# Kernel optimization log

Hardware: AMD Instinct MI355X
Metric: run time of the kernel (lower is better)

Reference implementation:

```python
import jax, jax.numpy as jnp
import numpy as np

N, D, M, H, FF, L = 8192, 14, 36, 256, 2048, 2  # rows, d_model, material feats, mlp hidden, ffn, layers
EPS = 1e-5


def _ln(x, g, b):
    mu = jnp.mean(x, axis=-1, keepdims=True)
    var = jnp.mean((x - mu) ** 2, axis=-1, keepdims=True)
    return (x - mu) * jax.lax.rsqrt(var + EPS) * g + b


def setup_inputs() -> dict:
    key = jax.random.key(0)
    ks = iter(jax.random.split(key, 32))
    p = lambda shape, fan: jax.random.normal(next(ks), shape, jnp.float32) * (fan ** -0.5)
    return {
        "x": jax.random.normal(next(ks), (N, D), jnp.float32),
        "y": jax.random.normal(next(ks), (N, M), jnp.float32),
        # 2 post-LN TransformerEncoderLayers (nhead=1, dim_feedforward=2048, relu)
        "attn_wqkv": p((L, 3 * D, D), D), "attn_bqkv": p((L, 3 * D), D),
        "attn_wo": p((L, D, D), D), "attn_bo": p((L, D), D),
        "ln1_g": jnp.ones((L, D)), "ln1_b": jnp.zeros((L, D)),
        "ff_w1": p((L, FF, D), D), "ff_b1": p((L, FF), D),
        "ff_w2": p((L, D, FF), FF), "ff_b2": p((L, D), FF),
        "ln2_g": jnp.ones((L, D)), "ln2_b": jnp.zeros((L, D)),
        "fc1_w": p((D, D), D), "fc1_b": p((D,), D),
        "fc2_w": p((1, D), D), "fc2_b": p((1,), D),
        "fc3_w": p((H, D + M + 1), D + M + 1), "fc3_b": p((H,), D + M + 1),
        "fc4_w": p((H, H), H), "fc4_b": p((H,), H),
        "fc5_w": p((1, H), H), "fc5_b": p((1,), H),
    }


def reference(x, y, attn_wqkv, attn_bqkv, attn_wo, attn_bo, ln1_g, ln1_b,
              ff_w1, ff_b1, ff_w2, ff_b2, ln2_g, ln2_b,
              fc1_w, fc1_b, fc2_w, fc2_b, fc3_w, fc3_b, fc4_w, fc4_b, fc5_w, fc5_b):
    h = x  # [N, D]; batch of size 1 squeezed away
    for l in range(L):
        qkv = h @ attn_wqkv[l].T + attn_bqkv[l]            # [N, 3D]
        q, k, v = jnp.split(qkv, 3, axis=-1)
        scores = (q @ k.T) * (D ** -0.5)                   # [N, N]
        a = jax.nn.softmax(scores, axis=-1) @ v            # [N, D]
        a = a @ attn_wo[l].T + attn_bo[l]
        h = _ln(h + a, ln1_g[l], ln1_b[l])
        f = jax.nn.relu(h @ ff_w1[l].T + ff_b1[l]) @ ff_w2[l].T + ff_b2[l]
        h = _ln(h + f, ln2_g[l], ln2_b[l])
    x1 = h @ fc1_w.T + fc1_b                               # [N, D]
    size_out = (x1 @ fc2_w.T + fc2_b)[:, 0]                # [N]

    # batched replacement of the per-row python loop
    size_int = size_out.astype(jnp.int32)                  # trunc toward zero, like .int()
    size_f = size_int.astype(jnp.float32)[:, None]         # [N, 1]
    reg_in = jnp.concatenate([size_f, x, y], axis=1)       # [N, 1+D+M]
    r = jax.nn.relu(reg_in @ fc3_w.T + fc3_b)
    r = jax.nn.relu(r @ fc4_w.T + fc4_b)
    reg_values = (r @ fc5_w.T + fc5_b)[:, 0]               # [N]
    reg_values = jnp.where(size_int != 0, reg_values, 0.0)
    return size_out, reg_values
```

## Files before the change

### kernel.cpp

```cpp
#include <hip/hip_runtime.h>
#include <math.h>

#define NN 8192
#define DD 14
#define DP 16
#define FF 2048
#define HID 256
#define LN_EPS 1e-5f
#define NCH 16
#define NFCH 8
#define QSCALE (1.4426950408889634f / 3.7416573867739413f)

typedef short bf16x8 __attribute__((ext_vector_type(8)));
typedef float f32x4 __attribute__((ext_vector_type(4)));

#define LOAD16(dst, srcp) { \
  const float4* _p = (const float4*)(srcp); \
  float4 _a = _p[0], _b = _p[1], _c = _p[2], _d = _p[3]; \
  dst[0]=_a.x; dst[1]=_a.y; dst[2]=_a.z; dst[3]=_a.w; \
  dst[4]=_b.x; dst[5]=_b.y; dst[6]=_b.z; dst[7]=_b.w; \
  dst[8]=_c.x; dst[9]=_c.y; dst[10]=_c.z; dst[11]=_c.w; \
  dst[12]=_d.x; dst[13]=_d.y; dst[14]=_d.z; dst[15]=_d.w; }

#define STORE16(dstp, src) { \
  float4* _p = (float4*)(dstp); \
  _p[0] = make_float4(src[0], src[1], src[2], src[3]); \
  _p[1] = make_float4(src[4], src[5], src[6], src[7]); \
  _p[2] = make_float4(src[8], src[9], src[10], src[11]); \
  _p[3] = make_float4(src[12], src[13], src[14], src[15]); }

static __device__ __forceinline__ float fast_exp2(float x) {
#if __has_builtin(__builtin_amdgcn_exp2f)
  return __builtin_amdgcn_exp2f(x);
#else
  return exp2f(x);
#endif
}

static __device__ __forceinline__ unsigned short bf_hi(float x) {
  return (unsigned short)(__float_as_uint(x) >> 16);
}
static __device__ __forceinline__ float bf_hi_f(float x) {
  return __uint_as_float(__float_as_uint(x) & 0xffff0000u);
}

static __device__ __forceinline__ void qkv_compute_store(
    int r, const float* hr, const float* __restrict__ wqkv,
    const float* __restrict__ bqkv, unsigned int* __restrict__ Qpack,
    unsigned int* __restrict__ KB1, unsigned int* __restrict__ KB2,
    unsigned short* __restrict__ VhiT, unsigned short* __restrict__ VloT) {
  float q[14], k[14], v[14];
  #pragma unroll 6
  for (int c = 0; c < 42; c++) {
    const float* w = wqkv + c * 14;
    float s = bqkv[c];
    #pragma unroll
    for (int d = 0; d < 14; d++) s = fmaf(hr[d], w[d], s);
    if (c < 14)       q[c] = s * QSCALE;
    else if (c < 28)  k[c - 14] = s;
    else              v[c - 28] = s;
  }
  unsigned int qp[16], k1[16], k2[16];
  unsigned short qh[14], ql[14], kh[14], kl[14];
  #pragma unroll
  for (int d = 0; d < 14; d++) {
    qh[d] = bf_hi(q[d]);
    ql[d] = bf_hi(q[d] - bf_hi_f(q[d]));
    kh[d] = bf_hi(k[d]);
    kl[d] = bf_hi(k[d] - bf_hi_f(k[d]));
  }
  #pragma unroll
  for (int i = 0; i < 7; i++) {
    qp[i]     = (unsigned int)qh[2*i] | ((unsigned int)qh[2*i+1] << 16);
    qp[8 + i] = (unsigned int)ql[2*i] | ((unsigned int)ql[2*i+1] << 16);
    k1[i]     = (unsigned int)kh[2*i] | ((unsigned int)kh[2*i+1] << 16);
    k1[8 + i] = k1[i];
    k2[i]     = (unsigned int)kl[2*i] | ((unsigned int)kl[2*i+1] << 16);
    k2[8 + i] = k2[i];
  }
  qp[7] = 0; qp[15] = 0; k1[7] = 0; k1[15] = 0; k2[7] = 0; k2[15] = 0;
  uint4* Qp4 = (uint4*)(Qpack + (size_t)r * 16);
  uint4* K14 = (uint4*)(KB1 + (size_t)r * 16);
  uint4* K24 = (uint4*)(KB2 + (size_t)r * 16);
  #pragma unroll
  for (int i = 0; i < 4; i++) {
    Qp4[i] = make_uint4(qp[4*i], qp[4*i+1], qp[4*i+2], qp[4*i+3]);
    K14[i] = make_uint4(k1[4*i], k1[4*i+1], k1[4*i+2], k1[4*i+3]);
    K24[i] = make_uint4(k2[4*i], k2[4*i+1], k2[4*i+2], k2[4*i+3]);
  }
  #pragma unroll
  for (int d = 0; d < 14; d++) {
    VhiT[(size_t)d * NN + r] = bf_hi(v[d]);
    VloT[(size_t)d * NN + r] = bf_hi(v[d] - bf_hi_f(v[d]));
  }
  VhiT[(size_t)14 * NN + r] = 0x3F80;
  VhiT[(size_t)15 * NN + r] = 0;
  VloT[(size_t)14 * NN + r] = 0;
  VloT[(size_t)15 * NN + r] = 0;
}

static __device__ __forceinline__ void store_apack(unsigned int* dst, const float* o) {
  unsigned int qp[16];
  unsigned short hh[14], ll[14];
  #pragma unroll
  for (int d = 0; d < 14; d++) {
    hh[d] = bf_hi(o[d]);
    ll[d] = bf_hi(o[d] - bf_hi_f(o[d]));
  }
  #pragma unroll
  for (int i = 0; i < 7; i++) {
    qp[i]     = (unsigned int)hh[2*i] | ((unsigned int)hh[2*i+1] << 16);
    qp[8 + i] = (unsigned int)ll[2*i] | ((unsigned int)ll[2*i+1] << 16);
  }
  qp[7] = 0; qp[15] = 0;
  uint4* d4 = (uint4*)dst;
  #pragma unroll
  for (int i = 0; i < 4; i++)
    d4[i] = make_uint4(qp[4*i], qp[4*i+1], qp[4*i+2], qp[4*i+3]);
}

__global__ void pack_weights(const float* __restrict__ w3, const float* __restrict__ w4,
                             const float* __restrict__ ffw1, const float* __restrict__ ffw2,
                             unsigned short* __restrict__ B3h, unsigned short* __restrict__ B3l,
                             unsigned short* __restrict__ B4h, unsigned short* __restrict__ B4l,
                             unsigned int* __restrict__ W1B1, unsigned int* __restrict__ W1B2,
                             unsigned short* __restrict__ W2h, unsigned short* __restrict__ W2l) {
  const int blk = blockIdx.x, tid = threadIdx.x;
  if (blk < 32) {
    int t = blk * 256 + tid;
    int lane = t & 63, ks = (t >> 6) & 7, nt = t >> 9;
    int n = nt * 16 + (lane & 15);
    int k0 = ks * 32 + (lane >> 4) * 8;
    unsigned int h4[4], l4[4];
    #pragma unroll
    for (int jj = 0; jj < 4; jj++) {
      unsigned short h2[2], l2[2];
      #pragma unroll
      for (int e = 0; e < 2; e++) {
        float v = w4[(size_t)n * 256 + k0 + jj * 2 + e];
        h2[e] = bf_hi(v);
        l2[e] = bf_hi(v - bf_hi_f(v));
      }
      h4[jj] = (unsigned int)h2[0] | ((unsigned int)h2[1] << 16);
      l4[jj] = (unsigned int)l2[0] | ((unsigned int)l2[1] << 16);
    }
    ((uint4*)B4h)[t] = make_uint4(h4[0], h4[1], h4[2], h4[3]);
    ((uint4*)B4l)[t] = make_uint4(l4[0], l4[1], l4[2], l4[3]);
    if (ks < 2) {
      int fi = (nt * 2 + ks) * 64 + lane;
      #pragma unroll
      for (int jj = 0; jj < 4; jj++) {
        unsigned short h2[2], l2[2];
        #pragma unroll
        for (int e = 0; e < 2; e++) {
          int k = k0 + jj * 2 + e;
          float v = (k < 51) ? w3[(size_t)n * 51 + k] : 0.f;
          h2[e] = bf_hi(v);
          l2[e] = bf_hi(v - bf_hi_f(v));
        }
        h4[jj] = (unsigned int)h2[0] | ((unsigned int)h2[1] << 16);
        l4[jj] = (unsigned int)l2[0] | ((unsigned int)l2[1] << 16);
      }
      ((uint4*)B3h)[fi] = make_uint4(h4[0], h4[1], h4[2], h4[3]);
      ((uint4*)B3l)[fi] = make_uint4(l4[0], l4[1], l4[2], l4[3]);
    }
  } else if (blk < 48) {
    int t = (blk - 32) * 256 + tid;
    int l = t >> 11, j = t & 2047;
    const float* wrow = ffw1 + ((size_t)l * FF + j) * 14;
    unsigned int k1[16], k2[16];
    unsigned short kh[14], kl[14];
    #pragma unroll
    for (int d = 0; d < 14; d++) {
      float v = wrow[d];
      kh[d] = bf_hi(v);
      kl[d] = bf_hi(v - bf_hi_f(v));
    }
    #pragma unroll
    for (int i = 0; i < 7; i++) {
      k1[i] = (unsigned int)kh[2*i] | ((unsigned int)kh[2*i+1] << 16);
      k1[8 + i] = k1[i];
      k2[i] = (unsigned int)kl[2*i] | ((unsigned int)kl[2*i+1] << 16);
      k2[8 + i] = k2[i];
    }
    k1[7] = 0; k1[15] = 0; k2[7] = 0; k2[15] = 0;
    uint4* d1 = (uint4*)(W1B1 + (size_t)t * 16);
    uint4* d2 = (uint4*)(W1B2 + (size_t)t * 16);
    #pragma unroll
    for (int i = 0; i < 4; i++) {
      d1[i] = make_uint4(k1[4*i], k1[4*i+1], k1[4*i+2], k1[4*i+3]);
      d2[i] = make_uint4(k2[4*i], k2[4*i+1], k2[4*i+2], k2[4*i+3]);
    }
  } else {
    int t = (blk - 48) * 256 + tid;
    int l = t >> 11, j = t & 2047;
    #pragma unroll
    for (int d = 0; d < 16; d++) {
      float v = (d < 14) ? ffw2[((size_t)l * 14 + d) * FF + j] : 0.f;
      W2h[((size_t)l * 16 + d) * FF + j] = bf_hi(v);
      W2l[((size_t)l * 16 + d) * FF + j] = bf_hi(v - bf_hi_f(v));
    }
  }
}

__global__ void qkv_pack_x(const float* __restrict__ x, const float* __restrict__ wqkv,
                           const float* __restrict__ bqkv, float* __restrict__ h,
                           unsigned int* __restrict__ Qpack,
                           unsigned int* __restrict__ KB1, unsigned int* __restrict__ KB2,
                           unsigned short* __restrict__ VhiT,
                           unsigned short* __restrict__ VloT) {
  int r = blockIdx.x * 64 + threadIdx.x;
  float hr[16];
  #pragma unroll
  for (int d = 0; d < 14; d++) hr[d] = x[(size_t)r * 14 + d];
  hr[14] = 0.f; hr[15] = 0.f;
  STORE16(h + (size_t)r * DP, hr);
  qkv_compute_store(r, hr, wqkv, bqkv, Qpack, KB1, KB2, VhiT, VloT);
}

__global__ __launch_bounds__(256, 4) void attn_mfma(
    const unsigned int* __restrict__ Qpack, const unsigned int* __restrict__ KB1,
    const unsigned int* __restrict__ KB2, const unsigned short* __restrict__ VhiT,
    const unsigned short* __restrict__ VloT, float* __restrict__ part) {
  __shared__ float Plds[4][16][36];
  const int tid = threadIdx.x;
  const int wave = tid >> 6;
  const int lane = tid & 63;
  const int lo4 = lane & 15;
  const int hi4 = lane >> 4;
  const int qbase = blockIdx.x * 128 + wave * 32;
  const int kbase0 = blockIdx.y * 512;

  const bf16x8* Qp = (const bf16x8*)Qpack;
  const bf16x8* B1 = (const bf16x8*)KB1;
  const bf16x8* B2 = (const bf16x8*)KB2;
  const bf16x8* Vh = (const bf16x8*)VhiT;
  const bf16x8* Vl = (const bf16x8*)VloT;

  bf16x8 aQ0 = Qp[(size_t)(qbase + lo4) * 4 + hi4];
  bf16x8 aQ1 = Qp[(size_t)(qbase + 16 + lo4) * 4 + hi4];
  f32x4 acc0 = {0.f, 0.f, 0.f, 0.f};
  f32x4 acc1 = {0.f, 0.f, 0.f, 0.f};
  const f32x4 zero = {0.f, 0.f, 0.f, 0.f};

  for (int c = 0; c < 16; c++) {
    const int kb = kbase0 + c * 32;
    bf16x8 b1g0 = B1[(size_t)(kb + lo4) * 4 + hi4];
    bf16x8 b2g0 = B2[(size_t)(kb + lo4) * 4 + hi4];
    bf16x8 b1g1 = B1[(size_t)(kb + 16 + lo4) * 4 + hi4];
    bf16x8 b2g1 = B2[(size_t)(kb + 16 + lo4) * 4 + hi4];
    bf16x8 vh = Vh[(size_t)lo4 * 1024 + (kb >> 3) + hi4];
    bf16x8 vl = Vl[(size_t)lo4 * 1024 + (kb >> 3) + hi4];

    #pragma unroll
    for (int sub = 0; sub < 2; sub++) {
      bf16x8 aQ = sub ? aQ1 : aQ0;
      f32x4 s0 = __builtin_amdgcn_mfma_f32_16x16x32_bf16(aQ, b1g0, zero, 0, 0, 0);
      s0 = __builtin_amdgcn_mfma_f32_16x16x32_bf16(aQ, b2g0, s0, 0, 0, 0);
      f32x4 s1 = __builtin_amdgcn_mfma_f32_16x16x32_bf16(aQ, b1g1, zero, 0, 0, 0);
      s1 = __builtin_amdgcn_mfma_f32_16x16x32_bf16(aQ, b2g1, s1, 0, 0, 0);
      #pragma unroll
      for (int reg = 0; reg < 4; reg++) {
        Plds[wave][hi4 * 4 + reg][lo4]      = fast_exp2(s0[reg]);
        Plds[wave][hi4 * 4 + reg][16 + lo4] = fast_exp2(s1[reg]);
      }
      __asm__ volatile("s_waitcnt lgkmcnt(0)" ::: "memory");
      const float4* pr = (const float4*)&Plds[wave][lo4][hi4 * 8];
      float4 f0 = pr[0];
      float4 f1 = pr[1];
      float pv[8] = {f0.x, f0.y, f0.z, f0.w, f1.x, f1.y, f1.z, f1.w};
      bf16x8 ph, pl;
      #pragma unroll
      for (int i = 0; i < 8; i++) {
        unsigned int u = __float_as_uint(pv[i]);
        ph[i] = (short)(u >> 16);
        float rr = pv[i] - __uint_as_float(u & 0xffff0000u);
        pl[i] = (short)(__float_as_uint(rr) >> 16);
      }
      f32x4 acc = sub ? acc1 : acc0;
      acc = __builtin_amdgcn_mfma_f32_16x16x32_bf16(ph, vh, acc, 0, 0, 0);
      acc = __builtin_amdgcn_mfma_f32_16x16x32_bf16(pl, vh, acc, 0, 0, 0);
      acc = __builtin_amdgcn_mfma_f32_16x16x32_bf16(ph, vl, acc, 0, 0, 0);
      if (sub) acc1 = acc; else acc0 = acc;
      __asm__ volatile("s_waitcnt lgkmcnt(0)" ::: "memory");
    }
  }
  float* pbase = part + (size_t)blockIdx.y * NN * 16;
  #pragma unroll
  for (int reg = 0; reg < 4; reg++) {
    int row0 = qbase + hi4 * 4 + reg;
    pbase[(size_t)row0 * 16 + lo4] = acc0[reg];
    pbase[(size_t)(row0 + 16) * 16 + lo4] = acc1[reg];
  }
}

__global__ void attn_comb_ln1(float* __restrict__ h, const float* __restrict__ part,
                              const float* __restrict__ wo, const float* __restrict__ bo,
                              const float* __restrict__ g, const float* __restrict__ b,
                              unsigned int* __restrict__ Hpack) {
  int r = blockIdx.x * 64 + threadIdx.x;
  float L = 0.f;
  float A[14];
  #pragma unroll
  for (int d = 0; d < 14; d++) A[d] = 0.f;
  for (int c = 0; c < NCH; c++) {
    float p[16];
    LOAD16(p, part + ((size_t)c * NN + r) * 16);
    L += p[14];
    #pragma unroll
    for (int d = 0; d < 14; d++) A[d] += p[d];
  }
  float inv = 1.f / L;
  float a[14];
  #pragma unroll
  for (int d = 0; d < 14; d++) a[d] = A[d] * inv;
  float hr[16];
  LOAD16(hr, h + (size_t)r * DP);
  float xx[14];
  #pragma unroll
  for (int i = 0; i < 14; i++) {
    float s = bo[i];
    #pragma unroll
    for (int d = 0; d < 14; d++) s = fmaf(wo[i * 14 + d], a[d], s);
    xx[i] = hr[i] + s;
  }
  float mu = 0.f;
  #pragma unroll
  for (int i = 0; i < 14; i++) mu += xx[i];
  mu *= (1.f / 14.f);
  float var = 0.f;
  #pragma unroll
  for (int i = 0; i < 14; i++) { float t = xx[i] - mu; var = fmaf(t, t, var); }
  var *= (1.f / 14.f);
  float rs = rsqrtf(var + LN_EPS);
  float o[16];
  #pragma unroll
  for (int i = 0; i < 14; i++) o[i] = fmaf((xx[i] - mu) * rs, g[i], b[i]);
  o[14] = 0.f; o[15] = 0.f;
  STORE16(h + (size_t)r * DP, o);
  store_apack(Hpack + (size_t)r * 16, o);
}

__global__ __launch_bounds__(256, 4) void ffn_mfma(
    const unsigned int* __restrict__ Hpack, const unsigned int* __restrict__ W1B1,
    const unsigned int* __restrict__ W1B2, const unsigned short* __restrict__ W2h,
    const unsigned short* __restrict__ W2l, const float* __restrict__ b1,
    float* __restrict__ part) {
  __shared__ float Plds[4][16][36];
  const int tid = threadIdx.x;
  const int wave = tid >> 6;
  const int lane = tid & 63;
  const int lo4 = lane & 15;
  const int hi4 = lane >> 4;
  const int qbase = blockIdx.x * 128 + wave * 32;
  const int jbase0 = blockIdx.y * 256;

  const bf16x8* Hp = (const bf16x8*)Hpack;
  const bf16x8* B1 = (const bf16x8*)W1B1;
  const bf16x8* B2 = (const bf16x8*)W1B2;
  const bf16x8* Vh = (const bf16x8*)W2h;
  const bf16x8* Vl = (const bf16x8*)W2l;

  bf16x8 aH0 = Hp[(size_t)(qbase + lo4) * 4 + hi4];
  bf16x8 aH1 = Hp[(size_t)(qbase + 16 + lo4) * 4 + hi4];
  f32x4 acc0 = {0.f, 0.f, 0.f, 0.f};
  f32x4 acc1 = {0.f, 0.f, 0.f, 0.f};
  const f32x4 zero = {0.f, 0.f, 0.f, 0.f};

  for (int c = 0; c < 8; c++) {
    const int jb = jbase0 + c * 32;
    bf16x8 b1g0 = B1[(size_t)(jb + lo4) * 4 + hi4];
    bf16x8 b2g0 = B2[(size_t)(jb + lo4) * 4 + hi4];
    bf16x8 b1g1 = B1[(size_t)(jb + 16 + lo4) * 4 + hi4];
    bf16x8 b2g1 = B2[(size_t)(jb + 16 + lo4) * 4 + hi4];
    bf16x8 vh = Vh[(size_t)lo4 * 256 + (jb >> 3) + hi4];
    bf16x8 vl = Vl[(size_t)lo4 * 256 + (jb >> 3) + hi4];
    float bb0 = b1[jb + lo4];
    float bb1 = b1[jb + 16 + lo4];

    #pragma unroll
    for (int sub = 0; sub < 2; sub++) {
      bf16x8 aH = sub ? aH1 : aH0;
      f32x4 s0 = __builtin_amdgcn_mfma_f32_16x16x32_bf16(aH, b1g0, zero, 0, 0, 0);
      s0 = __builtin_amdgcn_mfma_f32_16x16x32_bf16(aH, b2g0, s0, 0, 0, 0);
      f32x4 s1 = __builtin_amdgcn_mfma_f32_16x16x32_bf16(aH, b1g1, zero, 0, 0, 0);
      s1 = __builtin_amdgcn_mfma_f32_16x16x32_bf16(aH, b2g1, s1, 0, 0, 0);
      #pragma unroll
      for (int reg = 0; reg < 4; reg++) {
        Plds[wave][hi4 * 4 + reg][lo4]      = fmaxf(s0[reg] + bb0, 0.f);
        Plds[wave][hi4 * 4 + reg][16 + lo4] = fmaxf(s1[reg] + bb1, 0.f);
      }
      __asm__ volatile("s_waitcnt lgkmcnt(0)" ::: "memory");
      const float4* pr = (const float4*)&Plds[wave][lo4][hi4 * 8];
      float4 f0 = pr[0];
      float4 f1 = pr[1];
      float pv[8] = {f0.x, f0.y, f0.z, f0.w, f1.x, f1.y, f1.z, f1.w};
      bf16x8 th, tl;
      #pragma unroll
      for (int i = 0; i < 8; i++) {
        unsigned int u = __float_as_uint(pv[i]);
        th[i] = (short)(u >> 16);
        float rr = pv[i] - __uint_as_float(u & 0xffff0000u);
        tl[i] = (short)(__float_as_uint(rr) >> 16);
      }
      f32x4 acc = sub ? acc1 : acc0;
      acc = __builtin_amdgcn_mfma_f32_16x16x32_bf16(th, vh, acc, 0, 0, 0);
      acc = __builtin_amdgcn_mfma_f32_16x16x32_bf16(tl, vh, acc, 0, 0, 0);
      acc = __builtin_amdgcn_mfma_f32_16x16x32_bf16(th, vl, acc, 0, 0, 0);
      if (sub) acc1 = acc; else acc0 = acc;
      __asm__ volatile("s_waitcnt lgkmcnt(0)" ::: "memory");
    }
  }
  float* pbase = part + (size_t)blockIdx.y * NN * 16;
  #pragma unroll
  for (int reg = 0; reg < 4; reg++) {
    int row0 = qbase + hi4 * 4 + reg;
    pbase[(size_t)row0 * 16 + lo4] = acc0[reg];
    pbase[(size_t)(row0 + 16) * 16 + lo4] = acc1[reg];
  }
}

__global__ void ffn_ln2_qkv(float* __restrict__ h, const float* __restrict__ part,
                            const float* __restrict__ b2, const float* __restrict__ g,
                            const float* __restrict__ b,
                            const float* __restrict__ wqkv, const float* __restrict__ bqkv,
                            unsigned int* __restrict__ Qpack,
                            unsigned int* __restrict__ KB1, unsigned int* __restrict__ KB2,
                            unsigned short* __restrict__ VhiT,
                            unsigned short* __restrict__ VloT) {
  int r = blockIdx.x * 64 + threadIdx.x;
  float f[14];
  #pragma unroll
  for (int d = 0; d < 14; d++) f[d] = b2[d];
  for (int c = 0; c < NFCH; c++) {
    float p[16];
    LOAD16(p, part + ((size_t)c * NN + r) * 16);
    #pragma unroll
    for (int d = 0; d < 14; d++) f[d] += p[d];
  }
  float hr[16];
  LOAD16(hr, h + (size_t)r * DP);
  float xx[14];
  #pragma unroll
  for (int i = 0; i < 14; i++) xx[i] = hr[i] + f[i];
  float mu = 0.f;
  #pragma unroll
  for (int i = 0; i < 14; i++) mu += xx[i];
  mu *= (1.f / 14.f);
  float var = 0.f;
  #pragma unroll
  for (int i = 0; i < 14; i++) { float t = xx[i] - mu; var = fmaf(t, t, var); }
  var *= (1.f / 14.f);
  float rs = rsqrtf(var + LN_EPS);
  float o[16];
  #pragma unroll
  for (int i = 0; i < 14; i++) o[i] = fmaf((xx[i] - mu) * rs, g[i], b[i]);
  o[14] = 0.f; o[15] = 0.f;
  STORE16(h + (size_t)r * DP, o);
  qkv_compute_store(r, o, wqkv, bqkv, Qpack, KB1, KB2, VhiT, VloT);
}

__global__ void ffn_ln2_size(const float* __restrict__ h, const float* __restrict__ part,
                             const float* __restrict__ b2, const float* __restrict__ g,
                             const float* __restrict__ b,
                             const float* __restrict__ fc1w, const float* __restrict__ fc1b,
                             const float* __restrict__ fc2w, const float* __restrict__ fc2b,
                             float* __restrict__ out, float* __restrict__ sizef) {
  int r = blockIdx.x * 64 + threadIdx.x;
  float f[14];
  #pragma unroll
  for (int d = 0; d < 14; d++) f[d] = b2[d];
  for (int c = 0; c < NFCH; c++) {
    float p[16];
    LOAD16(p, part + ((size_t)c * NN + r) * 16);
    #pragma unroll
    for (int d = 0; d < 14; d++) f[d] += p[d];
  }
  float hr[16];
  LOAD16(hr, h + (size_t)r * DP);
  float xx[14];
  #pragma unroll
  for (int i = 0; i < 14; i++) xx[i] = hr[i] + f[i];
  float mu = 0.f;
  #pragma unroll
  for (int i = 0; i < 14; i++) mu += xx[i];
  mu *= (1.f / 14.f);
  float var = 0.f;
  #pragma unroll
  for (int i = 0; i < 14; i++) { float t = xx[i] - mu; var = fmaf(t, t, var); }
  var *= (1.f / 14.f);
  float rs = rsqrtf(var + LN_EPS);
  float o[14];
  #pragma unroll
  for (int i = 0; i < 14; i++) o[i] = fmaf((xx[i] - mu) * rs, g[i], b[i]);
  float s = fc2b[0];
  #pragma unroll
  for (int i = 0; i < 14; i++) {
    float t = fc1b[i];
    #pragma unroll
    for (int d = 0; d < 14; d++) t = fmaf(fc1w[i * 14 + d], o[d], t);
    s = fmaf(t, fc2w[i], s);
  }
  out[r] = s;
  int si = (int)s;
  sizef[r] = (float)si;
}

__global__ __launch_bounds__(256, 4) void head_reg_mfma(
    const float* __restrict__ x, const float* __restrict__ y,
    const float* __restrict__ sizef,
    const unsigned short* __restrict__ B3h, const unsigned short* __restrict__ B3l,
    const float* __restrict__ b3,
    const unsigned short* __restrict__ B4h, const unsigned short* __restrict__ B4l,
    const float* __restrict__ b4,
    const float* __restrict__ w5, const float* __restrict__ b5,
    float* __restrict__ outr) {
  __shared__ alignas(16) unsigned short Ah[16][72], Al[16][72];
  __shared__ alignas(16) unsigned short R1h[16][264], R1l[16][264];
  __shared__ float sred[4][16][16];
  const int tid = threadIdx.x;
  const int wave = tid >> 6;
  const int lane = tid & 63;
  const int lo4 = lane & 15;
  const int hi4 = lane >> 4;
  const int rbase = blockIdx.x * 16;

  for (int idx = tid; idx < 16 * 64; idx += 256) {
    int m = idx >> 6, k = idx & 63;
    int r = rbase + m;
    float v = 0.f;
    if (k == 0)       v = sizef[r];
    else if (k < 15)  v = x[(size_t)r * 14 + (k - 1)];
    else if (k < 51)  v = y[(size_t)r * 36 + (k - 15)];
    Ah[m][k] = bf_hi(v);
    Al[m][k] = bf_hi(v - bf_hi_f(v));
  }
  __syncthreads();

  const f32x4 zero = {0.f, 0.f, 0.f, 0.f};
  f32x4 acc[4];
  #pragma unroll
  for (int nt = 0; nt < 4; nt++) acc[nt] = zero;

  #pragma unroll
  for (int ks = 0; ks < 2; ks++) {
    bf16x8 ah = *(const bf16x8*)&Ah[lo4][ks * 32 + hi4 * 8];
    bf16x8 al = *(const bf16x8*)&Al[lo4][ks * 32 + hi4 * 8];
    #pragma unroll
    for (int nt = 0; nt < 4; nt++) {
      int fi = ((wave * 4 + nt) * 2 + ks) * 64 + lane;
      bf16x8 bh = ((const bf16x8*)B3h)[fi];
      bf16x8 bl = ((const bf16x8*)B3l)[fi];
      acc[nt] = __builtin_amdgcn_mfma_f32_16x16x32_bf16(ah, bh, acc[nt], 0, 0, 0);
      acc[nt] = __builtin_amdgcn_mfma_f32_16x16x32_bf16(al, bh, acc[nt], 0, 0, 0);
      acc[nt] = __builtin_amdgcn_mfma_f32_16x16x32_bf16(ah, bl, acc[nt], 0, 0, 0);
    }
  }
  #pragma unroll
  for (int nt = 0; nt < 4; nt++) {
    int n = (wave * 4 + nt) * 16 + lo4;
    float bb = b3[n];
    #pragma unroll
    for (int reg = 0; reg < 4; reg++) {
      int m = hi4 * 4 + reg;
      float v = fmaxf(acc[nt][reg] + bb, 0.f);
      R1h[m][n] = bf_hi(v);
      R1l[m][n] = bf_hi(v - bf_hi_f(v));
    }
  }
  __syncthreads();

  #pragma unroll
  for (int nt = 0; nt < 4; nt++) acc[nt] = zero;
  #pragma unroll
  for (int ks = 0; ks < 8; ks++) {
    bf16x8 ah = *(const bf16x8*)&R1h[lo4][ks * 32 + hi4 * 8];
    bf16x8 al = *(const bf16x8*)&R1l[lo4][ks * 32 + hi4 * 8];
    #pragma unroll
    for (int nt = 0; nt < 4; nt++) {
      int fi = ((wave * 4 + nt) * 8 + ks) * 64 + lane;
      bf16x8 bh = ((const bf16x8*)B4h)[fi];
      bf16x8 bl = ((const bf16x8*)B4l)[fi];
      acc[nt] = __builtin_amdgcn_mfma_f32_16x16x32_bf16(ah, bh, acc[nt], 0, 0, 0);
      acc[nt] = __builtin_amdgcn_mfma_f32_16x16x32_bf16(al, bh, acc[nt], 0, 0, 0);
      acc[nt] = __builtin_amdgcn_mfma_f32_16x16x32_bf16(ah, bl, acc[nt], 0, 0, 0);
    }
  }
  float s[4] = {0.f, 0.f, 0.f, 0.f};
  #pragma unroll
  for (int nt = 0; nt < 4; nt++) {
    int n = (wave * 4 + nt) * 16 + lo4;
    float bb = b4[n], ww = w5[n];
    #pragma unroll
    for (int reg = 0; reg < 4; reg++)
      s[reg] = fmaf(fmaxf(acc[nt][reg] + bb, 0.f), ww, s[reg]);
  }
  #pragma unroll
  for (int reg = 0; reg < 4; reg++) sred[wave][hi4 * 4 + reg][lo4] = s[reg];
  __syncthreads();

  if (tid < 16) {
    float t = b5[0];
    #pragma unroll
    for (int w = 0; w < 4; w++) {
      const float4* p = (const float4*)&sred[w][tid][0];
      float4 a0 = p[0], a1 = p[1], a2 = p[2], a3 = p[3];
      t += ((a0.x + a0.y) + (a0.z + a0.w)) + ((a1.x + a1.y) + (a1.z + a1.w)) +
           ((a2.x + a2.y) + (a2.z + a2.w)) + ((a3.x + a3.y) + (a3.z + a3.w));
    }
    float sz = sizef[rbase + tid];
    outr[rbase + tid] = (sz != 0.f) ? t : 0.f;
  }
}

extern "C" void kernel_launch(void* const* d_in, const int* in_sizes, int n_in,
                              void* d_out, int out_size, void* d_ws, size_t ws_size,
                              hipStream_t stream) {
  const float* x    = (const float*)d_in[0];
  const float* y    = (const float*)d_in[1];
  const float* wqkv = (const float*)d_in[2];
  const float* bqkv = (const float*)d_in[3];
  const float* wo   = (const float*)d_in[4];
  const float* bo   = (const float*)d_in[5];
  const float* ln1g = (const float*)d_in[6];
  const float* ln1b = (const float*)d_in[7];
  const float* ffw1 = (const float*)d_in[8];
  const float* ffb1 = (const float*)d_in[9];
  const float* ffw2 = (const float*)d_in[10];
  const float* ffb2 = (const float*)d_in[11];
  const float* ln2g = (const float*)d_in[12];
  const float* ln2b = (const float*)d_in[13];
  const float* fc1w = (const float*)d_in[14];
  const float* fc1b = (const float*)d_in[15];
  const float* fc2w = (const float*)d_in[16];
  const float* fc2b = (const float*)d_in[17];
  const float* fc3w = (const float*)d_in[18];
  const float* fc3b = (const float*)d_in[19];
  const float* fc4w = (const float*)d_in[20];
  const float* fc4b = (const float*)d_in[21];
  const float* fc5w = (const float*)d_in[22];
  const float* fc5b = (const float*)d_in[23];

  float* ws = (float*)d_ws;
  float*          h     = ws;
  unsigned int*   Qpack = (unsigned int*)(ws + 131072);
  unsigned int*   KB1   = (unsigned int*)(ws + 262144);
  unsigned int*   KB2   = (unsigned int*)(ws + 393216);
  unsigned short* VhiT  = (unsigned short*)(ws + 524288);
  unsigned short* VloT  = (unsigned short*)(ws + 589824);
  unsigned int*   Hpack = (unsigned int*)(ws + 655360);
  float*          part  = ws + 786432;
  float*          sizef = ws + 2883584;
  unsigned short* B3h   = (unsigned short*)(ws + 2891776);
  unsigned short* B3l   = (unsigned short*)(ws + 2899968);
  unsigned short* B4h   = (unsigned short*)(ws + 2908160);
  unsigned short* B4l   = (unsigned short*)(ws + 2940928);
  unsigned int*   W1B1  = (unsigned int*)(ws + 2973696);
  unsigned int*   W1B2  = (unsigned int*)(ws + 3039232);
  unsigned short* W2h   = (unsigned short*)(ws + 3104768);
  unsigned short* W2l   = (unsigned short*)(ws + 3137536);

  float* out = (float*)d_out;

  pack_weights<<<64, 256, 0, stream>>>(fc3w, fc4w, ffw1, ffw2, B3h, B3l, B4h, B4l,
                                       W1B1, W1B2, W2h, W2l);
  qkv_pack_x<<<128, 64, 0, stream>>>(x, wqkv, bqkv, h, Qpack, KB1, KB2, VhiT, VloT);
  for (int l = 0; l < 2; l++) {
    attn_mfma<<<dim3(64, NCH), 256, 0, stream>>>(Qpack, KB1, KB2, VhiT, VloT, part);
    attn_comb_ln1<<<128, 64, 0, stream>>>(h, part, wo + (size_t)l * 196,
                                          bo + (size_t)l * 14, ln1g + (size_t)l * 14,
                                          ln1b + (size_t)l * 14, Hpack);
    ffn_mfma<<<dim3(64, NFCH), 256, 0, stream>>>(
        Hpack, W1B1 + (size_t)l * 2048 * 16, W1B2 + (size_t)l * 2048 * 16,
        W2h + (size_t)l * 16 * FF, W2l + (size_t)l * 16 * FF,
        ffb1 + (size_t)l * FF, part);
    if (l == 0) {
      ffn_ln2_qkv<<<128, 64, 0, stream>>>(h, part, ffb2, ln2g, ln2b,
                                          wqkv + 42 * 14, bqkv + 42,
                                          Qpack, KB1, KB2, VhiT, VloT);
    } else {
      ffn_ln2_size<<<128, 64, 0, stream>>>(h, part, ffb2 + 14, ln2g + 14, ln2b + 14,
                                           fc1w, fc1b, fc2w, fc2b, out, sizef);
    }
  }
  head_reg_mfma<<<512, 256, 0, stream>>>(x, y, sizef, B3h, B3l, fc3b, B4h, B4l, fc4b,
                                         fc5w, fc5b, out + NN);
}
```

Before: 261.6 us.

## Fuse pack kernels, interleave MFMA sub-tiles, split combine reductions, fuse tail

Merges weight packing with the initial QKV projection into one launch, and fuses the final LN2/size head into the regression head kernel, which removes launches and the sizef round trip through global memory. The attention and FFN inner loops now issue both 16-row sub-tiles' MFMAs together with a larger LDS staging buffer, so independent MFMA chains overlap instead of running in a serial loop. The combine/LN kernels now use four threads per row with shuffle reductions over the partial chunks, giving more parallelism at the cost of idle lanes in the per-row tail. The extra LDS and registers may reduce occupancy.

```diff
diff --git a/kernel.cpp b/kernel.cpp
--- a/kernel.cpp
+++ b/kernel.cpp
@@ -42,6 +42,16 @@
 }
 static __device__ __forceinline__ float bf_hi_f(float x) {
   return __uint_as_float(__float_as_uint(x) & 0xffff0000u);
+}
+
+static __device__ __forceinline__ void split8(const float* pv, bf16x8* ph, bf16x8* pl) {
+  #pragma unroll
+  for (int i = 0; i < 8; i++) {
+    unsigned int u = __float_as_uint(pv[i]);
+    (*ph)[i] = (short)(u >> 16);
+    float rr = pv[i] - __uint_as_float(u & 0xffff0000u);
+    (*pl)[i] = (short)(__float_as_uint(rr) >> 16);
+  }
 }
 
 static __device__ __forceinline__ void qkv_compute_store(
@@ -119,12 +129,17 @@
     d4[i] = make_uint4(qp[4*i], qp[4*i+1], qp[4*i+2], qp[4*i+3]);
 }
 
-__global__ void pack_weights(const float* __restrict__ w3, const float* __restrict__ w4,
-                             const float* __restrict__ ffw1, const float* __restrict__ ffw2,
-                             unsigned short* __restrict__ B3h, unsigned short* __restrict__ B3l,
-                             unsigned short* __restrict__ B4h, unsigned short* __restrict__ B4l,
-                             unsigned int* __restrict__ W1B1, unsigned int* __restrict__ W1B2,
-                             unsigned short* __restrict__ W2h, unsigned short* __restrict__ W2l) {
+__global__ void pack_all(const float* __restrict__ w3, const float* __restrict__ w4,
+                         const float* __restrict__ ffw1, const float* __restrict__ ffw2,
+                         const float* __restrict__ x, const float* __restrict__ wqkv,
+                         const float* __restrict__ bqkv, float* __restrict__ h,
+                         unsigned int* __restrict__ Qpack,
+                         unsigned int* __restrict__ KB1, unsigned int* __restrict__ KB2,
+                         unsigned short* __restrict__ VhiT, unsigned short* __restrict__ VloT,
+                         unsigned short* __restrict__ B3h, unsigned short* __restrict__ B3l,
+                         unsigned short* __restrict__ B4h, unsigned short* __restrict__ B4l,
+                         unsigned int* __restrict__ W1B1, unsigned int* __restrict__ W1B2,
+                         unsigned short* __restrict__ W2h, unsigned short* __restrict__ W2l) {
   const int blk = blockIdx.x, tid = threadIdx.x;
   if (blk < 32) {
     int t = blk * 256 + tid;
@@ -191,7 +206,7 @@
       d1[i] = make_uint4(k1[4*i], k1[4*i+1], k1[4*i+2], k1[4*i+3]);
       d2[i] = make_uint4(k2[4*i], k2[4*i+1], k2[4*i+2], k2[4*i+3]);
     }
-  } else {
+  } else if (blk < 64) {
     int t = (blk - 48) * 256 + tid;
     int l = t >> 11, j = t & 2047;
     #pragma unroll
@@ -200,29 +215,22 @@
       W2h[((size_t)l * 16 + d) * FF + j] = bf_hi(v);
       W2l[((size_t)l * 16 + d) * FF + j] = bf_hi(v - bf_hi_f(v));
     }
-  }
-}
-
-__global__ void qkv_pack_x(const float* __restrict__ x, const float* __restrict__ wqkv,
-                           const float* __restrict__ bqkv, float* __restrict__ h,
-                           unsigned int* __restrict__ Qpack,
-                           unsigned int* __restrict__ KB1, unsigned int* __restrict__ KB2,
-                           unsigned short* __restrict__ VhiT,
-                           unsigned short* __restrict__ VloT) {
-  int r = blockIdx.x * 64 + threadIdx.x;
-  float hr[16];
-  #pragma unroll
-  for (int d = 0; d < 14; d++) hr[d] = x[(size_t)r * 14 + d];
-  hr[14] = 0.f; hr[15] = 0.f;
-  STORE16(h + (size_t)r * DP, hr);
-  qkv_compute_store(r, hr, wqkv, bqkv, Qpack, KB1, KB2, VhiT, VloT);
+  } else {
+    int r = (blk - 64) * 256 + tid;
+    float hr[16];
+    #pragma unroll
+    for (int d = 0; d < 14; d++) hr[d] = x[(size_t)r * 14 + d];
+    hr[14] = 0.f; hr[15] = 0.f;
+    STORE16(h + (size_t)r * DP, hr);
+    qkv_compute_store(r, hr, wqkv, bqkv, Qpack, KB1, KB2, VhiT, VloT);
+  }
 }
 
 __global__ __launch_bounds__(256, 4) void attn_mfma(
     const unsigned int* __restrict__ Qpack, const unsigned int* __restrict__ KB1,
     const unsigned int* __restrict__ KB2, const unsigned short* __restrict__ VhiT,
     const unsigned short* __restrict__ VloT, float* __restrict__ part) {
-  __shared__ float Plds[4][16][36];
+  __shared__ float Plds[4][32][36];
   const int tid = threadIdx.x;
   const int wave = tid >> 6;
   const int lane = tid & 63;
@@ -252,38 +260,37 @@
     bf16x8 vh = Vh[(size_t)lo4 * 1024 + (kb >> 3) + hi4];
     bf16x8 vl = Vl[(size_t)lo4 * 1024 + (kb >> 3) + hi4];
 
-    #pragma unroll
-    for (int sub = 0; sub < 2; sub++) {
-      bf16x8 aQ = sub ? aQ1 : aQ0;
-      f32x4 s0 = __builtin_amdgcn_mfma_f32_16x16x32_bf16(aQ, b1g0, zero, 0, 0, 0);
-      s0 = __builtin_amdgcn_mfma_f32_16x16x32_bf16(aQ, b2g0, s0, 0, 0, 0);
-      f32x4 s1 = __builtin_amdgcn_mfma_f32_16x16x32_bf16(aQ, b1g1, zero, 0, 0, 0);
-      s1 = __builtin_amdgcn_mfma_f32_16x16x32_bf16(aQ, b2g1, s1, 0, 0, 0);
-      #pragma unroll
-      for (int reg = 0; reg < 4; reg++) {
-        Plds[wave][hi4 * 4 + reg][lo4]      = fast_exp2(s0[reg]);
-        Plds[wave][hi4 * 4 + reg][16 + lo4] = fast_exp2(s1[reg]);
-      }
-      __asm__ volatile("s_waitcnt lgkmcnt(0)" ::: "memory");
-      const float4* pr = (const float4*)&Plds[wave][lo4][hi4 * 8];
-      float4 f0 = pr[0];
-      float4 f1 = pr[1];
-      float pv[8] = {f0.x, f0.y, f0.z, f0.w, f1.x, f1.y, f1.z, f1.w};
-      bf16x8 ph, pl;
-      #pragma unroll
-      for (int i = 0; i < 8; i++) {
-        unsigned int u = __float_as_uint(pv[i]);
-        ph[i] = (short)(u >> 16);
-        float rr = pv[i] - __uint_as_float(u & 0xffff0000u);
-        pl[i] = (short)(__float_as_uint(rr) >> 16);
-      }
-      f32x4 acc = sub ? acc1 : acc0;
-      acc = __builtin_amdgcn_mfma_f32_16x16x32_bf16(ph, vh, acc, 0, 0, 0);
-      acc = __builtin_amdgcn_mfma_f32_16x16x32_bf16(pl, vh, acc, 0, 0, 0);
-      acc = __builtin_amdgcn_mfma_f32_16x16x32_bf16(ph, vl, acc, 0, 0, 0);
-      if (sub) acc1 = acc; else acc0 = acc;
-      __asm__ volatile("s_waitcnt lgkmcnt(0)" ::: "memory");
-    }
+    f32x4 s00 = __builtin_amdgcn_mfma_f32_16x16x32_bf16(aQ0, b1g0, zero, 0, 0, 0);
+    f32x4 s01 = __builtin_amdgcn_mfma_f32_16x16x32_bf16(aQ0, b1g1, zero, 0, 0, 0);
+    f32x4 s10 = __builtin_amdgcn_mfma_f32_16x16x32_bf16(aQ1, b1g0, zero, 0, 0, 0);
+    f32x4 s11 = __builtin_amdgcn_mfma_f32_16x16x32_bf16(aQ1, b1g1, zero, 0, 0, 0);
+    s00 = __builtin_amdgcn_mfma_f32_16x16x32_bf16(aQ0, b2g0, s00, 0, 0, 0);
+    s01 = __builtin_amdgcn_mfma_f32_16x16x32_bf16(aQ0, b2g1, s01, 0, 0, 0);
+    s10 = __builtin_amdgcn_mfma_f32_16x16x32_bf16(aQ1, b2g0, s10, 0, 0, 0);
+    s11 = __builtin_amdgcn_mfma_f32_16x16x32_bf16(aQ1, b2g1, s11, 0, 0, 0);
+    #pragma unroll
+    for (int reg = 0; reg < 4; reg++) {
+      Plds[wave][hi4 * 4 + reg][lo4]           = fast_exp2(s00[reg]);
+      Plds[wave][hi4 * 4 + reg][16 + lo4]      = fast_exp2(s01[reg]);
+      Plds[wave][16 + hi4 * 4 + reg][lo4]      = fast_exp2(s10[reg]);
+      Plds[wave][16 + hi4 * 4 + reg][16 + lo4] = fast_exp2(s11[reg]);
+    }
+    __asm__ volatile("s_waitcnt lgkmcnt(0)" ::: "memory");
+    const float4* p0 = (const float4*)&Plds[wave][lo4][hi4 * 8];
+    const float4* p1 = (const float4*)&Plds[wave][16 + lo4][hi4 * 8];
+    float4 a0 = p0[0], a1 = p0[1], c0 = p1[0], c1 = p1[1];
+    float pv0[8] = {a0.x, a0.y, a0.z, a0.w, a1.x, a1.y, a1.z, a1.w};
+    float pv1[8] = {c0.x, c0.y, c0.z, c0.w, c1.x, c1.y, c1.z, c1.w};
+    bf16x8 ph0, pl0, ph1, pl1;
+    split8(pv0, &ph0, &pl0);
+    split8(pv1, &ph1, &pl1);
+    acc0 = __builtin_amdgcn_mfma_f32_16x16x32_bf16(ph0, vh, acc0, 0, 0, 0);
+    acc1 = __builtin_amdgcn_mfma_f32_16x16x32_bf16(ph1, vh, acc1, 0, 0, 0);
+    acc0 = __builtin_amdgcn_mfma_f32_16x16x32_bf16(pl0, vh, acc0, 0, 0, 0);
+    acc1 = __builtin_amdgcn_mfma_f32_16x16x32_bf16(pl1, vh, acc1, 0, 0, 0);
+    acc0 = __builtin_amdgcn_mfma_f32_16x16x32_bf16(ph0, vl, acc0, 0, 0, 0);
+    acc1 = __builtin_amdgcn_mfma_f32_16x16x32_bf16(ph1, vl, acc1, 0, 0, 0);
+    __asm__ volatile("s_waitcnt lgkmcnt(0)" ::: "memory");
   }
   float* pbase = part + (size_t)blockIdx.y * NN * 16;
   #pragma unroll
@@ -298,47 +305,57 @@
                               const float* __restrict__ wo, const float* __restrict__ bo,
                               const float* __restrict__ g, const float* __restrict__ b,
                               unsigned int* __restrict__ Hpack) {
-  int r = blockIdx.x * 64 + threadIdx.x;
+  int t = blockIdx.x * 128 + threadIdx.x;
+  int r = t >> 2, q = t & 3;
   float L = 0.f;
   float A[14];
   #pragma unroll
   for (int d = 0; d < 14; d++) A[d] = 0.f;
-  for (int c = 0; c < NCH; c++) {
+  #pragma unroll
+  for (int c = q; c < NCH; c += 4) {
     float p[16];
     LOAD16(p, part + ((size_t)c * NN + r) * 16);
     L += p[14];
     #pragma unroll
     for (int d = 0; d < 14; d++) A[d] += p[d];
   }
-  float inv = 1.f / L;
-  float a[14];
-  #pragma unroll
-  for (int d = 0; d < 14; d++) a[d] = A[d] * inv;
-  float hr[16];
-  LOAD16(hr, h + (size_t)r * DP);
-  float xx[14];
-  #pragma unroll
-  for (int i = 0; i < 14; i++) {
-    float s = bo[i];
-    #pragma unroll
-    for (int d = 0; d < 14; d++) s = fmaf(wo[i * 14 + d], a[d], s);
-    xx[i] = hr[i] + s;
-  }
-  float mu = 0.f;
-  #pragma unroll
-  for (int i = 0; i < 14; i++) mu += xx[i];
-  mu *= (1.f / 14.f);
-  float var = 0.f;
-  #pragma unroll
-  for (int i = 0; i < 14; i++) { float t = xx[i] - mu; var = fmaf(t, t, var); }
-  var *= (1.f / 14.f);
-  float rs = rsqrtf(var + LN_EPS);
-  float o[16];
-  #pragma unroll
-  for (int i = 0; i < 14; i++) o[i] = fmaf((xx[i] - mu) * rs, g[i], b[i]);
-  o[14] = 0.f; o[15] = 0.f;
-  STORE16(h + (size_t)r * DP, o);
-  store_apack(Hpack + (size_t)r * 16, o);
+  #pragma unroll
+  for (int off = 1; off < 4; off <<= 1) {
+    L += __shfl_xor(L, off, 64);
+    #pragma unroll
+    for (int d = 0; d < 14; d++) A[d] += __shfl_xor(A[d], off, 64);
+  }
+  if (q == 0) {
+    float inv = 1.f / L;
+    float a[14];
+    #pragma unroll
+    for (int d = 0; d < 14; d++) a[d] = A[d] * inv;
+    float hr[16];
+    LOAD16(hr, h + (size_t)r * DP);
+    float xx[14];
+    #pragma unroll
+    for (int i = 0; i < 14; i++) {
+      float s = bo[i];
+      #pragma unroll
+      for (int d = 0; d < 14; d++) s = fmaf(wo[i * 14 + d], a[d], s);
+      xx[i] = hr[i] + s;
+    }
+    float mu = 0.f;
+    #pragma unroll
+    for (int i = 0; i < 14; i++) mu += xx[i];
+    mu *= (1.f / 14.f);
+    float var = 0.f;
+    #pragma unroll
+    for (int i = 0; i < 14; i++) { float tt = xx[i] - mu; var = fmaf(tt, tt, var); }
+    var *= (1.f / 14.f);
+    float rs = rsqrtf(var + LN_EPS);
+    float o[16];
+    #pragma unroll
+    for (int i = 0; i < 14; i++) o[i] = fmaf((xx[i] - mu) * rs, g[i], b[i]);
+    o[14] = 0.f; o[15] = 0.f;
+    STORE16(h + (size_t)r * DP, o);
+    store_apack(Hpack + (size_t)r * 16, o);
+  }
 }
 
 __global__ __launch_bounds__(256, 4) void ffn_mfma(
@@ -346,7 +363,7 @@
     const unsigned int* __restrict__ W1B2, const unsigned short* __restrict__ W2h,
     const unsigned short* __restrict__ W2l, const float* __restrict__ b1,
     float* __restrict__ part) {
-  __shared__ float Plds[4][16][36];
+  __shared__ float Plds[4][32][36];
   const int tid = threadIdx.x;
   const int wave = tid >> 6;
   const int lane = tid & 63;
@@ -378,38 +395,37 @@
     float bb0 = b1[jb + lo4];
     float bb1 = b1[jb + 16 + lo4];
 
-    #pragma unroll
-    for (int sub = 0; sub < 2; sub++) {
-      bf16x8 aH = sub ? aH1 : aH0;
-      f32x4 s0 = __builtin_amdgcn_mfma_f32_16x16x32_bf16(aH, b1g0, zero, 0, 0, 0);
-      s0 = __builtin_amdgcn_mfma_f32_16x16x32_bf16(aH, b2g0, s0, 0, 0, 0);
-      f32x4 s1 = __builtin_amdgcn_mfma_f32_16x16x32_bf16(aH, b1g1, zero, 0, 0, 0);
-      s1 = __builtin_amdgcn_mfma_f32_16x16x32_bf16(aH, b2g1, s1, 0, 0, 0);
-      #pragma unroll
-      for (int reg = 0; reg < 4; reg++) {
-        Plds[wave][hi4 * 4 + reg][lo4]      = fmaxf(s0[reg] + bb0, 0.f);
-        Plds[wave][hi4 * 4 + reg][16 + lo4] = fmaxf(s1[reg] + bb1, 0.f);
-      }
-      __asm__ volatile("s_waitcnt lgkmcnt(0)" ::: "memory");
-      const float4* pr = (const float4*)&Plds[wave][lo4][hi4 * 8];
-      float4 f0 = pr[0];
-      float4 f1 = pr[1];
-      float pv[8] = {f0.x, f0.y, f0.z, f0.w, f1.x, f1.y, f1.z, f1.w};
-      bf16x8 th, tl;
-      #pragma unroll
-      for (int i = 0; i < 8; i++) {
-        unsigned int u = __float_as_uint(pv[i]);
-        th[i] = (short)(u >> 16);
-        float rr = pv[i] - __uint_as_float(u & 0xffff0000u);
-        tl[i] = (short)(__float_as_uint(rr) >> 16);
-      }
-      f32x4 acc = sub ? acc1 : acc0;
-      acc = __builtin_amdgcn_mfma_f32_16x16x32_bf16(th, vh, acc, 0, 0, 0);
-      acc = __builtin_amdgcn_mfma_f32_16x16x32_bf16(tl, vh, acc, 0, 0, 0);
-      acc = __builtin_amdgcn_mfma_f32_16x16x32_bf16(th, vl, acc, 0, 0, 0);
-      if (sub) acc1 = acc; else acc0 = acc;
-      __asm__ volatile("s_waitcnt lgkmcnt(0)" ::: "memory");
-    }
+    f32x4 s00 = __builtin_amdgcn_mfma_f32_16x16x32_bf16(aH0, b1g0, zero, 0, 0, 0);
+    f32x4 s01 = __builtin_amdgcn_mfma_f32_16x16x32_bf16(aH0, b1g1, zero, 0, 0, 0);
+    f32x4 s10 = __builtin_amdgcn_mfma_f32_16x16x32_bf16(aH1, b1g0, zero, 0, 0, 0);
+    f32x4 s11 = __builtin_amdgcn_mfma_f32_16x16x32_bf16(aH1, b1g1, zero, 0, 0, 0);
+    s00 = __builtin_amdgcn_mfma_f32_16x16x32_bf16(aH0, b2g0, s00, 0, 0, 0);
+    s01 = __builtin_amdgcn_mfma_f32_16x16x32_bf16(aH0, b2g1, s01, 0, 0, 0);
+    s10 = __builtin_amdgcn_mfma_f32_16x16x32_bf16(aH1, b2g0, s10, 0, 0, 0);
+    s11 = __builtin_amdgcn_mfma_f32_16x16x32_bf16(aH1, b2g1, s11, 0, 0, 0);
+    #pragma unroll
+    for (int reg = 0; reg < 4; reg++) {
+      Plds[wave][hi4 * 4 + reg][lo4]           = fmaxf(s00[reg] + bb0, 0.f);
+      Plds[wave][hi4 * 4 + reg][16 + lo4]      = fmaxf(s01[reg] + bb1, 0.f);
+      Plds[wave][16 + hi4 * 4 + reg][lo4]      = fmaxf(s10[reg] + bb0, 0.f);
+      Plds[wave][16 + hi4 * 4 + reg][16 + lo4] = fmaxf(s11[reg] + bb1, 0.f);
+    }
+    __asm__ volatile("s_waitcnt lgkmcnt(0)" ::: "memory");
+    const float4* p0 = (const float4*)&Plds[wave][lo4][hi4 * 8];
+    const float4* p1 = (const float4*)&Plds[wave][16 + lo4][hi4 * 8];
+    float4 a0 = p0[0], a1 = p0[1], c0 = p1[0], c1 = p1[1];
+    float pv0[8] = {a0.x, a0.y, a0.z, a0.w, a1.x, a1.y, a1.z, a1.w};
+    float pv1[8] = {c0.x, c0.y, c0.z, c0.w, c1.x, c1.y, c1.z, c1.w};
+    bf16x8 th0, tl0, th1, tl1;
+    split8(pv0, &th0, &tl0);
+    split8(pv1, &th1, &tl1);
+    acc0 = __builtin_amdgcn_mfma_f32_16x16x32_bf16(th0, vh, acc0, 0, 0, 0);
+    acc1 = __builtin_amdgcn_mfma_f32_16x16x32_bf16(th1, vh, acc1, 0, 0, 0);
+    acc0 = __builtin_amdgcn_mfma_f32_16x16x32_bf16(tl0, vh, acc0, 0, 0, 0);
+    acc1 = __builtin_amdgcn_mfma_f32_16x16x32_bf16(tl1, vh, acc1, 0, 0, 0);
+    acc0 = __builtin_amdgcn_mfma_f32_16x16x32_bf16(th0, vl, acc0, 0, 0, 0);
+    acc1 = __builtin_amdgcn_mfma_f32_16x16x32_bf16(th1, vl, acc1, 0, 0, 0);
+    __asm__ volatile("s_waitcnt lgkmcnt(0)" ::: "memory");
   }
   float* pbase = part + (size_t)blockIdx.y * NN * 16;
   #pragma unroll
@@ -428,96 +444,63 @@
                             unsigned int* __restrict__ KB1, unsigned int* __restrict__ KB2,
                             unsigned short* __restrict__ VhiT,
                             unsigned short* __restrict__ VloT) {
-  int r = blockIdx.x * 64 + threadIdx.x;
+  int t = blockIdx.x * 128 + threadIdx.x;
+  int r = t >> 2, q = t & 3;
   float f[14];
   #pragma unroll
-  for (int d = 0; d < 14; d++) f[d] = b2[d];
-  for (int c = 0; c < NFCH; c++) {
+  for (int d = 0; d < 14; d++) f[d] = 0.f;
+  #pragma unroll
+  for (int c = q; c < NFCH; c += 4) {
     float p[16];
     LOAD16(p, part + ((size_t)c * NN + r) * 16);
     #pragma unroll
     for (int d = 0; d < 14; d++) f[d] += p[d];
   }
-  float hr[16];
-  LOAD16(hr, h + (size_t)r * DP);
-  float xx[14];
-  #pragma unroll
-  for (int i = 0; i < 14; i++) xx[i] = hr[i] + f[i];
-  float mu = 0.f;
-  #pragma unroll
-  for (int i = 0; i < 14; i++) mu += xx[i];
-  mu *= (1.f / 14.f);
-  float var = 0.f;
-  #pragma unroll
-  for (int i = 0; i < 14; i++) { float t = xx[i] - mu; var = fmaf(t, t, var); }
-  var *= (1.f / 14.f);
-  float rs = rsqrtf(var + LN_EPS);
-  float o[16];
-  #pragma unroll
-  for (int i = 0; i < 14; i++) o[i] = fmaf((xx[i] - mu) * rs, g[i], b[i]);
-  o[14] = 0.f; o[15] = 0.f;
-  STORE16(h + (size_t)r * DP, o);
-  qkv_compute_store(r, o, wqkv, bqkv, Qpack, KB1, KB2, VhiT, VloT);
-}
-
-__global__ void ffn_ln2_size(const float* __restrict__ h, const float* __restrict__ part,
-                             const float* __restrict__ b2, const float* __restrict__ g,
-                             const float* __restrict__ b,
-                             const float* __restrict__ fc1w, const float* __restrict__ fc1b,
-                             const float* __restrict__ fc2w, const float* __restrict__ fc2b,
-                             float* __restrict__ out, float* __restrict__ sizef) {
-  int r = blockIdx.x * 64 + threadIdx.x;
-  float f[14];
-  #pragma unroll
-  for (int d = 0; d < 14; d++) f[d] = b2[d];
-  for (int c = 0; c < NFCH; c++) {
-    float p[16];
-    LOAD16(p, part + ((size_t)c * NN + r) * 16);
-    #pragma unroll
-    for (int d = 0; d < 14; d++) f[d] += p[d];
-  }
-  float hr[16];
-  LOAD16(hr, h + (size_t)r * DP);
-  float xx[14];
-  #pragma unroll
-  for (int i = 0; i < 14; i++) xx[i] = hr[i] + f[i];
-  float mu = 0.f;
-  #pragma unroll
-  for (int i = 0; i < 14; i++) mu += xx[i];
-  mu *= (1.f / 14.f);
-  float var = 0.f;
-  #pragma unroll
-  for (int i = 0; i < 14; i++) { float t = xx[i] - mu; var = fmaf(t, t, var); }
-  var *= (1.f / 14.f);
-  float rs = rsqrtf(var + LN_EPS);
-  float o[14];
-  #pragma unroll
-  for (int i = 0; i < 14; i++) o[i] = fmaf((xx[i] - mu) * rs, g[i], b[i]);
-  float s = fc2b[0];
-  #pragma unroll
-  for (int i = 0; i < 14; i++) {
-    float t = fc1b[i];
-    #pragma unroll
-    for (int d = 0; d < 14; d++) t = fmaf(fc1w[i * 14 + d], o[d], t);
-    s = fmaf(t, fc2w[i], s);
-  }
-  out[r] = s;
-  int si = (int)s;
-  sizef[r] = (float)si;
-}
-
-__global__ __launch_bounds__(256, 4) void head_reg_mfma(
+  #pragma unroll
+  for (int off = 1; off < 4; off <<= 1) {
+    #pragma unroll
+    for (int d = 0; d < 14; d++) f[d] += __shfl_xor(f[d], off, 64);
+  }
+  if (q == 0) {
+    float hr[16];
+    LOAD16(hr, h + (size_t)r * DP);
+    float xx[14];
+    #pragma unroll
+    for (int i = 0; i < 14; i++) xx[i] = hr[i] + f[i] + b2[i];
+    float mu = 0.f;
+    #pragma unroll
+    for (int i = 0; i < 14; i++) mu += xx[i];
+    mu *= (1.f / 14.f);
+    float var = 0.f;
+    #pragma unroll
+    for (int i = 0; i < 14; i++) { float tt = xx[i] - mu; var = fmaf(tt, tt, var); }
+    var *= (1.f / 14.f);
+    float rs = rsqrtf(var + LN_EPS);
+    float o[16];
+    #pragma unroll
+    for (int i = 0; i < 14; i++) o[i] = fmaf((xx[i] - mu) * rs, g[i], b[i]);
+    o[14] = 0.f; o[15] = 0.f;
+    STORE16(h + (size_t)r * DP, o);
+    qkv_compute_store(r, o, wqkv, bqkv, Qpack, KB1, KB2, VhiT, VloT);
+  }
+}
+
+__global__ __launch_bounds__(256, 4) void tail_fused(
+    const float* __restrict__ h, const float* __restrict__ part,
+    const float* __restrict__ b2, const float* __restrict__ g, const float* __restrict__ b,
+    const float* __restrict__ fc1w, const float* __restrict__ fc1b,
+    const float* __restrict__ fc2w, const float* __restrict__ fc2b,
     const float* __restrict__ x, const float* __restrict__ y,
-    const float* __restrict__ sizef,
     const unsigned short* __restrict__ B3h, const unsigned short* __restrict__ B3l,
     const float* __restrict__ b3,
     const unsigned short* __restrict__ B4h, const unsigned short* __restrict__ B4l,
     const float* __restrict__ b4,
     const float* __restrict__ w5, const float* __restrict__ b5,
-    float* __restrict__ outr) {
+    float* __restrict__ out, float* __restrict__ outr) {
   __shared__ alignas(16) unsigned short Ah[16][72], Al[16][72];
   __shared__ alignas(16) unsigned short R1h[16][264], R1l[16][264];
   __shared__ float sred[4][16][16];
+  __shared__ float szf[16];
   const int tid = threadIdx.x;
   const int wave = tid >> 6;
   const int lane = tid & 63;
@@ -525,11 +508,57 @@
   const int hi4 = lane >> 4;
   const int rbase = blockIdx.x * 16;
 
+  if (tid < 128) {
+    int m = tid >> 3, c = tid & 7;
+    int r = rbase + m;
+    float p[16];
+    LOAD16(p, part + ((size_t)c * NN + r) * 16);
+    float f[14];
+    #pragma unroll
+    for (int d = 0; d < 14; d++) f[d] = p[d];
+    #pragma unroll
+    for (int off = 1; off < 8; off <<= 1) {
+      #pragma unroll
+      for (int d = 0; d < 14; d++) f[d] += __shfl_xor(f[d], off, 64);
+    }
+    if (c == 0) {
+      float hr[16];
+      LOAD16(hr, h + (size_t)r * DP);
+      float xx[14];
+      #pragma unroll
+      for (int i = 0; i < 14; i++) xx[i] = hr[i] + f[i] + b2[i];
+      float mu = 0.f;
+      #pragma unroll
+      for (int i = 0; i < 14; i++) mu += xx[i];
+      mu *= (1.f / 14.f);
+      float var = 0.f;
+      #pragma unroll
+      for (int i = 0; i < 14; i++) { float tt = xx[i] - mu; var = fmaf(tt, tt, var); }
+      var *= (1.f / 14.f);
+      float rs = rsqrtf(var + LN_EPS);
+      float o[14];
+      #pragma unroll
+      for (int i = 0; i < 14; i++) o[i] = fmaf((xx[i] - mu) * rs, g[i], b[i]);
+      float s = fc2b[0];
+      #pragma unroll
+      for (int i = 0; i < 14; i++) {
+        float tt = fc1b[i];
+        #pragma unroll
+        for (int d = 0; d < 14; d++) tt = fmaf(fc1w[i * 14 + d], o[d], tt);
+        s = fmaf(tt, fc2w[i], s);
+      }
+      out[r] = s;
+      int si = (int)s;
+      szf[m] = (float)si;
+    }
+  }
+  __syncthreads();
+
   for (int idx = tid; idx < 16 * 64; idx += 256) {
     int m = idx >> 6, k = idx & 63;
     int r = rbase + m;
     float v = 0.f;
-    if (k == 0)       v = sizef[r];
+    if (k == 0)       v = szf[m];
     else if (k < 15)  v = x[(size_t)r * 14 + (k - 1)];
     else if (k < 51)  v = y[(size_t)r * 36 + (k - 15)];
     Ah[m][k] = bf_hi(v);
@@ -608,7 +637,7 @@
       t += ((a0.x + a0.y) + (a0.z + a0.w)) + ((a1.x + a1.y) + (a1.z + a1.w)) +
            ((a2.x + a2.y) + (a2.z + a2.w)) + ((a3.x + a3.y) + (a3.z + a3.w));
     }
-    float sz = sizef[rbase + tid];
+    float sz = szf[tid];
     outr[rbase + tid] = (sz != 0.f) ? t : 0.f;
   }
 }
@@ -650,7 +679,6 @@
   unsigned short* VloT  = (unsigned short*)(ws + 589824);
   unsigned int*   Hpack = (unsigned int*)(ws + 655360);
   float*          part  = ws + 786432;
-  float*          sizef = ws + 2883584;
   unsigned short* B3h   = (unsigned short*)(ws + 2891776);
   unsigned short* B3l   = (unsigned short*)(ws + 2899968);
   unsigned short* B4h   = (unsigned short*)(ws + 2908160);
@@ -662,27 +690,26 @@
 
   float* out = (float*)d_out;
 
-  pack_weights<<<64, 256, 0, stream>>>(fc3w, fc4w, ffw1, ffw2, B3h, B3l, B4h, B4l,
-                                       W1B1, W1B2, W2h, W2l);
-  qkv_pack_x<<<128, 64, 0, stream>>>(x, wqkv, bqkv, h, Qpack, KB1, KB2, VhiT, VloT);
+  pack_all<<<96, 256, 0, stream>>>(fc3w, fc4w, ffw1, ffw2, x, wqkv, bqkv, h,
+                                   Qpack, KB1, KB2, VhiT, VloT,
+                                   B3h, B3l, B4h, B4l, W1B1, W1B2, W2h, W2l);
   for (int l = 0; l < 2; l++) {
     attn_mfma<<<dim3(64, NCH), 256, 0, stream>>>(Qpack, KB1, KB2, VhiT, VloT, part);
-    attn_comb_ln1<<<128, 64, 0, stream>>>(h, part, wo + (size_t)l * 196,
-                                          bo + (size_t)l * 14, ln1g + (size_t)l * 14,
-                                          ln1b + (size_t)l * 14, Hpack);
+    attn_comb_ln1<<<256, 128, 0, stream>>>(h, part, wo + (size_t)l * 196,
+                                           bo + (size_t)l * 14, ln1g + (size_t)l * 14,
+                                           ln1b + (size_t)l * 14, Hpack);
     ffn_mfma<<<dim3(64, NFCH), 256, 0, stream>>>(
         Hpack, W1B1 + (size_t)l * 2048 * 16, W1B2 + (size_t)l * 2048 * 16,
         W2h + (size_t)l * 16 * FF, W2l + (size_t)l * 16 * FF,
         ffb1 + (size_t)l * FF, part);
     if (l == 0) {
-      ffn_ln2_qkv<<<128, 64, 0, stream>>>(h, part, ffb2, ln2g, ln2b,
-                                          wqkv + 42 * 14, bqkv + 42,
-                                          Qpack, KB1, KB2, VhiT, VloT);
-    } else {
-      ffn_ln2_size<<<128, 64, 0, stream>>>(h, part, ffb2 + 14, ln2g + 14, ln2b + 14,
-                                           fc1w, fc1b, fc2w, fc2b, out, sizef);
-    }
-  }
-  head_reg_mfma<<<512, 256, 0, stream>>>(x, y, sizef, B3h, B3l, fc3b, B4h, B4l, fc4b,
-                                         fc5w, fc5b, out + NN);
-}
+      ffn_ln2_qkv<<<256, 128, 0, stream>>>(h, part, ffb2, ln2g, ln2b,
+                                           wqkv + 42 * 14, bqkv + 42,
+                                           Qpack, KB1, KB2, VhiT, VloT);
+    }
+  }
+  tail_fused<<<512, 256, 0, stream>>>(h, part, ffb2 + 14, ln2g + 14, ln2b + 14,
+                                      fc1w, fc1b, fc2w, fc2b, x, y,
+                                      B3h, B3l, fc3b, B4h, B4l, fc4b,
+                                      fc5w, fc5b, out, out + NN);
+}
```

Measured after the change: 255.6 us. -2.3%, faster.
